# Optimization experiments

Hardware: AMD Instinct MI355X
Metric: run time of the kernel (lower is better)

Reference implementation:

```python
import jax, jax.numpy as jnp
import numpy as np

DIM = 192
HEADS = 8
TIME = 256
HID = int(DIM * 2.66)  # 510
B, H, W = 4, 128, 128


def conv1x1(x, w, b):
    # w: [O, C], pointwise conv as einsum
    return jnp.einsum('bchw,oc->bohw', x, w) + b[None, :, None, None]


def dwconv3(x, w, b):
    # depthwise 3x3, w: [C, 1, 3, 3]
    y = jax.lax.conv_general_dilated(
        x, w, window_strides=(1, 1), padding='SAME',
        feature_group_count=x.shape[1],
        dimension_numbers=('NCHW', 'OIHW', 'NCHW'))
    return y + b[None, :, None, None]


def layernorm(x, w, b, eps=1e-6):
    # channel-wise LN; torch .std() is unbiased (ddof=1)
    C = x.shape[1]
    mean = x.mean(axis=1, keepdims=True)
    var = ((x - mean) ** 2).sum(axis=1, keepdims=True) / (C - 1)
    std = jnp.sqrt(var)
    return w * (x - mean) / (std + eps) + b


def modulate(x, t_emb, tw, tb):
    # time_mlp = Linear(SiLU(t_emb)); scale/shift conditioning
    t = jax.nn.silu(t_emb) @ tw.T + tb  # [B, 2C]
    scale, shift = jnp.split(t, 2, axis=-1)
    return x * (1.0 + scale[:, :, None, None]) + shift[:, :, None, None]


def l2norm(x, eps=1e-12):
    n = jnp.sqrt((x * x).sum(axis=-1, keepdims=True))
    return x / jnp.maximum(n, eps)


def mdta(x, t_emb, temp, qkv_w, qkv_b, dw_w, dw_b, proj_w, proj_b, tw, tb):
    Bn, C, Hh, Ww = x.shape
    x = modulate(x, t_emb, tw, tb)
    qkv = dwconv3(conv1x1(x, qkv_w, qkv_b), dw_w, dw_b)
    q, k, v = jnp.split(qkv, 3, axis=1)
    rs = lambda a: a.reshape(Bn, HEADS, C // HEADS, Hh * Ww)
    q, k, v = l2norm(rs(q)), l2norm(rs(k)), rs(v)
    attn = jnp.einsum('bhcl,bhdl->bhcd', q, k) * temp[None]  # [B,h,c,c]
    attn = jax.nn.softmax(attn, axis=-1)
    out = jnp.einsum('bhcd,bhdl->bhcl', attn, v).reshape(Bn, C, Hh, Ww)
    return conv1x1(out, proj_w, proj_b)


def gdfn(x, t_emb, c1_w, c1_b, dw_w, dw_b, c2_w, c2_b, tw, tb):
    x = modulate(x, t_emb, tw, tb)
    x = dwconv3(conv1x1(x, c1_w, c1_b), dw_w, dw_b)
    x1, x2 = jnp.split(x, 2, axis=1)
    return conv1x1(x1 * x2, c2_w, c2_b)


def setup_inputs() -> dict:
    key = jax.random.key(0)
    ks = jax.random.split(key, 16)
    s = 0.02
    d = {
        'x': jax.random.normal(ks[0], (B, DIM, H, W), jnp.float32),
        't_emb': jax.random.normal(ks[1], (B, TIME), jnp.float32),
        'n1_w': jnp.ones((1, DIM, 1, 1), jnp.float32),
        'n1_b': jnp.zeros((1, DIM, 1, 1), jnp.float32),
        'temp': jnp.ones((HEADS, 1, 1), jnp.float32),
        'a_qkv_w': jax.random.normal(ks[2], (3 * DIM, DIM), jnp.float32) * s,
        'a_qkv_b': jnp.zeros((3 * DIM,), jnp.float32),
        'a_dw_w': jax.random.normal(ks[3], (3 * DIM, 1, 3, 3), jnp.float32) * s,
        'a_dw_b': jnp.zeros((3 * DIM,), jnp.float32),
        'a_proj_w': jax.random.normal(ks[4], (DIM, DIM), jnp.float32) * s,
        'a_proj_b': jnp.zeros((DIM,), jnp.float32),
        'a_t_w': jax.random.normal(ks[5], (2 * DIM, TIME), jnp.float32) * s,
        'a_t_b': jnp.zeros((2 * DIM,), jnp.float32),
        'n2_w': jnp.ones((1, DIM, 1, 1), jnp.float32),
        'n2_b': jnp.zeros((1, DIM, 1, 1), jnp.float32),
        'f_c1_w': jax.random.normal(ks[6], (2 * HID, DIM), jnp.float32) * s,
        'f_c1_b': jnp.zeros((2 * HID,), jnp.float32),
        'f_dw_w': jax.random.normal(ks[7], (2 * HID, 1, 3, 3), jnp.float32) * s,
        'f_dw_b': jnp.zeros((2 * HID,), jnp.float32),
        'f_c2_w': jax.random.normal(ks[8], (DIM, HID), jnp.float32) * s,
        'f_c2_b': jnp.zeros((DIM,), jnp.float32),
        'f_t_w': jax.random.normal(ks[9], (2 * DIM, TIME), jnp.float32) * s,
        'f_t_b': jnp.zeros((2 * DIM,), jnp.float32),
    }
    return d


def reference(x, t_emb, n1_w, n1_b, temp, a_qkv_w, a_qkv_b, a_dw_w, a_dw_b,
              a_proj_w, a_proj_b, a_t_w, a_t_b, n2_w, n2_b,
              f_c1_w, f_c1_b, f_dw_w, f_dw_b, f_c2_w, f_c2_b, f_t_w, f_t_b):
    x = x + mdta(layernorm(x, n1_w, n1_b), t_emb, temp,
                 a_qkv_w, a_qkv_b, a_dw_w, a_dw_b, a_proj_w, a_proj_b, a_t_w, a_t_b)
    x = x + gdfn(layernorm(x, n2_w, n2_b), t_emb,
                 f_c1_w, f_c1_b, f_dw_w, f_dw_b, f_c2_w, f_c2_b, f_t_w, f_t_b)
    return x
```

## Files before the change

### kernel.cpp

```cpp
#include <hip/hip_runtime.h>
#include <math.h>

#define HW 16384

using short8 = __attribute__((ext_vector_type(8))) short;
using f32x4  = __attribute__((ext_vector_type(4))) float;

__device__ __forceinline__ float bf2f(unsigned short u){
  union { unsigned int i; float f; } x; x.i = ((unsigned int)u) << 16; return x.f;
}
__device__ __forceinline__ unsigned short f2bf(float f){
  union { float f; unsigned int i; } x; x.f = f;
  return (unsigned short)((x.i + 0x7FFFu + ((x.i >> 16) & 1u)) >> 16);
}

__global__ void castw_k(const float* __restrict__ in, unsigned short* __restrict__ out, int n){
  int i = blockIdx.x * 256 + threadIdx.x;
  if (i < n) out[i] = f2bf(in[i]);
}
__global__ void castw_pad_k(const float* __restrict__ in, unsigned short* __restrict__ out,
                            int M, int Kin, int Kout){
  int i = blockIdx.x * 256 + threadIdx.x;
  if (i < M * Kout){
    int m = i / Kout, k = i - m * Kout;
    out[i] = (k < Kin) ? f2bf(in[m * Kin + k]) : (unsigned short)0;
  }
}

__global__ void modk(const float* __restrict__ t_emb,
                     const float* __restrict__ aw, const float* __restrict__ ab,
                     const float* __restrict__ fw, const float* __restrict__ fb,
                     float* __restrict__ mod_a, float* __restrict__ mod_f){
  int o = blockIdx.x * 128 + threadIdx.x;
  int b = blockIdx.y;
  const float* w  = blockIdx.z ? fw : aw;
  const float* bi = blockIdx.z ? fb : ab;
  float* outp     = blockIdx.z ? mod_f : mod_a;
  const float* te = t_emb + b * 256;
  float acc = bi[o];
  for (int k = 0; k < 256; ++k){
    float u = te[k];
    float s = u / (1.f + expf(-u));
    acc += s * w[o * 256 + k];
  }
  outp[b * 384 + o] = acc;
}

__global__ __launch_bounds__(256) void lnmod_k(const float* __restrict__ x,
                                               const float* __restrict__ nw, const float* __restrict__ nb,
                                               const float* __restrict__ mod, unsigned short* __restrict__ y){
  int b = blockIdx.y;
  int p = blockIdx.x * 256 + threadIdx.x;
  const float* xb = x + (size_t)b * 192 * HW + p;
  float s = 0.f, s2 = 0.f;
  #pragma unroll 8
  for (int c = 0; c < 192; ++c){
    float v = xb[(size_t)c * HW]; s += v; s2 += v * v;
  }
  float mean = s * (1.f / 192.f);
  float var  = (s2 - s * mean) * (1.f / 191.f);
  float rinv = 1.f / (sqrtf(fmaxf(var, 0.f)) + 1e-6f);
  const float* mo = mod + b * 384;
  unsigned short* yb = y + ((size_t)b * HW + p) * 192;
  #pragma unroll
  for (int c8 = 0; c8 < 24; ++c8){
    unsigned short ob[8];
    #pragma unroll
    for (int j = 0; j < 8; ++j){
      int c = c8 * 8 + j;
      float v = xb[(size_t)c * HW];
      float ln = nw[c] * ((v - mean) * rinv) + nb[c];
      ob[j] = f2bf(ln * (1.f + mo[c]) + mo[192 + c]);
    }
    *(uint4*)(yb + c8 * 8) = *(const uint4*)ob;
  }
}

__global__ __launch_bounds__(256, 2) void gemm_tn2(const unsigned short* __restrict__ A,
                                                   const unsigned short* __restrict__ Bact,
                                                   const float* __restrict__ bias,
                                                   const float* resid, void* outp,
                                                   int M, int K, int nMb, int ofp32){
  const int N = HW;
  __shared__ unsigned short SMEM[20480];
  const int G = gridDim.x;
  const int bid = blockIdx.x;
  const int lb = (bid & 7) * (G >> 3) + (bid >> 3);
  const int mb = lb % nMb;
  const int rest = lb / nMb;
  const int n0 = (rest & 63) * 256;
  const int bz = rest >> 6;
  const unsigned short* Bp = Bact + (size_t)bz * N * K;
  const int m0 = mb * 64;
  const int t = threadIdx.x;
  const int w = t >> 6, lane = t & 63;
  const int l16 = lane & 15, quad = lane >> 4;

  const int arow = t >> 2, akc = t & 3;
  int gm = m0 + arow; if (gm > M - 1) gm = M - 1;
  const unsigned short* agp = A + (size_t)gm * K + akc * 8;
  const int aoff = arow * 32 + ((akc ^ ((arow ^ (arow >> 2)) & 3)) * 8);
  const int brow = t >> 2, bkc = t & 3;
  const unsigned short* bgp = Bp + (size_t)(n0 + brow) * K + bkc * 8;
  const int bslot = (bkc ^ ((brow ^ (brow >> 2)) & 3)) * 8;

  f32x4 acc[4][4];
  #pragma unroll
  for (int i = 0; i < 4; ++i)
    #pragma unroll
    for (int j = 0; j < 4; ++j) acc[i][j] = (f32x4){0.f, 0.f, 0.f, 0.f};

  const int kTiles = K >> 5;
  {
    uint4 va = *(const uint4*)agp;
    *(uint4*)&SMEM[aoff] = va;
    #pragma unroll
    for (int i = 0; i < 4; ++i){
      uint4 vb = *(const uint4*)(bgp + (size_t)(64 * i) * K);
      *(uint4*)&SMEM[4096 + (brow + 64 * i) * 32 + bslot] = vb;
    }
  }
  __syncthreads();

  const int fs = (quad ^ ((l16 ^ (l16 >> 2)) & 3)) * 8;
  for (int kt = 0; kt < kTiles; ++kt){
    const int cur = kt & 1;
    const bool more = (kt + 1 < kTiles);
    uint4 va; uint4 vb[4];
    if (more){
      const int k0 = (kt + 1) * 32;
      va = *(const uint4*)(agp + k0);
      #pragma unroll
      for (int i = 0; i < 4; ++i)
        vb[i] = *(const uint4*)(bgp + (size_t)(64 * i) * K + k0);
    }
    const int abase = cur * 2048;
    const int bbase = 4096 + cur * 8192;
    short8 af[4], bfr[4];
    #pragma unroll
    for (int mt = 0; mt < 4; ++mt)
      af[mt] = *(const short8*)&SMEM[abase + (mt * 16 + l16) * 32 + fs];
    #pragma unroll
    for (int nt = 0; nt < 4; ++nt)
      bfr[nt] = *(const short8*)&SMEM[bbase + (w * 64 + nt * 16 + l16) * 32 + fs];
    #pragma unroll
    for (int nt = 0; nt < 4; ++nt)
      #pragma unroll
      for (int mt = 0; mt < 4; ++mt)
        acc[mt][nt] = __builtin_amdgcn_mfma_f32_16x16x32_bf16(af[mt], bfr[nt], acc[mt][nt], 0, 0, 0);
    if (more){
      const int nabase = (cur ^ 1) * 2048;
      const int nbbase = 4096 + (cur ^ 1) * 8192;
      *(uint4*)&SMEM[nabase + aoff] = va;
      #pragma unroll
      for (int i = 0; i < 4; ++i)
        *(uint4*)&SMEM[nbbase + (brow + 64 * i) * 32 + bslot] = vb[i];
    }
    __syncthreads();
  }

  if (!ofp32){
    unsigned short* T = SMEM;
    #pragma unroll
    for (int mt = 0; mt < 4; ++mt)
      #pragma unroll
      for (int nt = 0; nt < 4; ++nt)
        #pragma unroll
        for (int r = 0; r < 4; ++r){
          int ml = mt * 16 + quad * 4 + r;
          int bm = m0 + ml; if (bm > M - 1) bm = M - 1;
          T[ml * 264 + w * 64 + nt * 16 + l16] = f2bf(acc[mt][nt][r] + bias[bm]);
        }
    __syncthreads();
    unsigned short* ob = (unsigned short*)outp + (size_t)bz * M * N;
    #pragma unroll
    for (int i = 0; i < 8; ++i){
      int c = t + 256 * i;
      int row = c >> 5, col = (c & 31) * 8;
      if (m0 + row < M)
        *(uint4*)(ob + (size_t)(m0 + row) * N + n0 + col) = *(const uint4*)&T[row * 264 + col];
    }
  } else {
    float* T = (float*)&SMEM[0];
    float* ob = (float*)outp + (size_t)bz * M * N;
    const float* rb = resid ? resid + (size_t)bz * M * N : nullptr;
    #pragma unroll
    for (int half = 0; half < 2; ++half){
      #pragma unroll
      for (int mt = 0; mt < 2; ++mt)
        #pragma unroll
        for (int nt = 0; nt < 4; ++nt)
          #pragma unroll
          for (int r = 0; r < 4; ++r){
            int ml = mt * 16 + quad * 4 + r;
            T[ml * 260 + w * 64 + nt * 16 + l16] = acc[half * 2 + mt][nt][r];
          }
      __syncthreads();
      #pragma unroll
      for (int i = 0; i < 8; ++i){
        int c = t + 256 * i;
        int row = c >> 6, col = (c & 63) * 4;
        int m = m0 + half * 32 + row;
        if (m < M){
          size_t idx = (size_t)m * N + n0 + col;
          f32x4 v = *(const f32x4*)&T[row * 260 + col];
          float bv = bias[m];
          v[0] += bv; v[1] += bv; v[2] += bv; v[3] += bv;
          if (rb){
            v[0] += rb[idx]; v[1] += rb[idx + 1]; v[2] += rb[idx + 2]; v[3] += rb[idx + 3];
          }
          *(f32x4*)&ob[idx] = v;
        }
      }
      __syncthreads();
    }
  }
}

__global__ __launch_bounds__(256) void dw3_k(const unsigned short* __restrict__ in,
                                             const float* __restrict__ w, const float* __restrict__ bias,
                                             unsigned short* __restrict__ out, int C,
                                             float* __restrict__ qn, float* __restrict__ kn){
  __shared__ unsigned short tile[66 * 128];
  __shared__ float red[4];
  int zc = blockIdx.y;
  int b = zc / C, c = zc - b * C;
  int r0 = blockIdx.x * 64;
  const unsigned short* im = in + ((size_t)(b * C + c)) * HW;
  unsigned short* om = out + ((size_t)(b * C + c)) * HW;
  int t = threadIdx.x;
  #pragma unroll
  for (int i = 0; i < 5; ++i){
    int idx = t + 256 * i;
    if (idx < 1056){
      int lr = idx >> 4, lc = (idx & 15) * 8;
      int gr = r0 - 1 + lr;
      uint4 v = {0u, 0u, 0u, 0u};
      if ((unsigned)gr < 128u) v = *(const uint4*)(im + gr * 128 + lc);
      *(uint4*)&tile[lr * 128 + lc] = v;
    }
  }
  __syncthreads();
  const float* wc = w + c * 9;
  float W[9];
  #pragma unroll
  for (int i = 0; i < 9; ++i) W[i] = wc[i];
  float bs = bias[c];
  float ssq = 0.f;
  #pragma unroll
  for (int i = 0; i < 4; ++i){
    int seg = t + 256 * i;
    int orow = seg >> 4, sc = (seg & 15) * 8;
    float acc[8];
    #pragma unroll
    for (int j = 0; j < 8; ++j) acc[j] = bs;
    #pragma unroll
    for (int rr = 0; rr < 3; ++rr){
      const unsigned short* rp = &tile[(orow + rr) * 128 + sc];
      float v[10];
      v[0] = (sc > 0) ? bf2f(rp[-1]) : 0.f;
      uint4 m = *(const uint4*)rp;
      const unsigned short* mu = (const unsigned short*)&m;
      #pragma unroll
      for (int j = 0; j < 8; ++j) v[j + 1] = bf2f(mu[j]);
      v[9] = (sc < 120) ? bf2f(rp[8]) : 0.f;
      float wa = W[rr * 3], wb = W[rr * 3 + 1], wd = W[rr * 3 + 2];
      #pragma unroll
      for (int j = 0; j < 8; ++j) acc[j] += wa * v[j] + wb * v[j + 1] + wd * v[j + 2];
    }
    unsigned short ob[8];
    #pragma unroll
    for (int j = 0; j < 8; ++j){
      ob[j] = f2bf(acc[j]);
      float q = bf2f(ob[j]);
      ssq += q * q;
    }
    *(uint4*)(om + (r0 + orow) * 128 + sc) = *(uint4*)ob;
  }
  if (c < 384){
    #pragma unroll
    for (int off = 32; off; off >>= 1) ssq += __shfl_down(ssq, off);
    if ((t & 63) == 0) red[t >> 6] = ssq;
    __syncthreads();
    if (t == 0){
      float s = red[0] + red[1] + red[2] + red[3];
      float* dst = (c < 192) ? (qn + b * 192 + c) : (kn + b * 192 + c - 192);
      atomicAdd(dst, s);
    }
  }
}

__global__ __launch_bounds__(256) void dwgate_k(const unsigned short* __restrict__ h,
                                                const float* __restrict__ w, const float* __restrict__ bias,
                                                unsigned short* __restrict__ g){
  __shared__ unsigned short tile[2 * 66 * 128];
  int zc = blockIdx.y;
  int b = zc / 510, j = zc - b * 510;
  int r0 = blockIdx.x * 64;
  const unsigned short* im1 = h + ((size_t)(b * 1020 + j)) * HW;
  const unsigned short* im2 = h + ((size_t)(b * 1020 + 510 + j)) * HW;
  int t = threadIdx.x;
  #pragma unroll
  for (int i = 0; i < 9; ++i){
    int idx = t + 256 * i;
    if (idx < 2112){
      int img = (idx >= 1056) ? 1 : 0;
      int li = idx - img * 1056;
      int lr = li >> 4, lc = (li & 15) * 8;
      int gr = r0 - 1 + lr;
      uint4 v = {0u, 0u, 0u, 0u};
      const unsigned short* im = img ? im2 : im1;
      if ((unsigned)gr < 128u) v = *(const uint4*)(im + gr * 128 + lc);
      *(uint4*)&tile[img * 8448 + lr * 128 + lc] = v;
    }
  }
  __syncthreads();
  float W1[9], W2[9];
  #pragma unroll
  for (int i = 0; i < 9; ++i){ W1[i] = w[j * 9 + i]; W2[i] = w[(510 + j) * 9 + i]; }
  float b1 = bias[j], b2 = bias[510 + j];
  unsigned short* gm = g + ((size_t)(b * 510 + j)) * HW;
  #pragma unroll
  for (int i = 0; i < 4; ++i){
    int seg = t + 256 * i;
    int orow = seg >> 4, sc = (seg & 15) * 8;
    float a1[8], a2[8];
    #pragma unroll
    for (int q = 0; q < 8; ++q){ a1[q] = b1; a2[q] = b2; }
    #pragma unroll
    for (int rr = 0; rr < 3; ++rr){
      #pragma unroll
      for (int img = 0; img < 2; ++img){
        const unsigned short* rp = &tile[img * 8448 + (orow + rr) * 128 + sc];
        float v[10];
        v[0] = (sc > 0) ? bf2f(rp[-1]) : 0.f;
        uint4 m = *(const uint4*)rp;
        const unsigned short* mu = (const unsigned short*)&m;
        #pragma unroll
        for (int q = 0; q < 8; ++q) v[q + 1] = bf2f(mu[q]);
        v[9] = (sc < 120) ? bf2f(rp[8]) : 0.f;
        const float* ww = img ? W2 : W1;
        float* aa = img ? a2 : a1;
        float wa = ww[rr * 3], wb = ww[rr * 3 + 1], wd = ww[rr * 3 + 2];
        #pragma unroll
        for (int q = 0; q < 8; ++q) aa[q] += wa * v[q] + wb * v[q + 1] + wd * v[q + 2];
      }
    }
    unsigned short ob[8];
    #pragma unroll
    for (int q = 0; q < 8; ++q) ob[q] = f2bf(a1[q] * a2[q]);
    *(uint4*)(gm + (r0 + orow) * 128 + sc) = *(uint4*)ob;
  }
}

__global__ __launch_bounds__(256) void tr_k(const unsigned short* __restrict__ in,
                                            unsigned short* __restrict__ out, int C, int Kout){
  __shared__ unsigned short tile[64 * 72];
  int b = blockIdx.z;
  int p0 = blockIdx.x * 64, c0 = blockIdx.y * 64;
  int t = threadIdx.x;
  #pragma unroll
  for (int i = 0; i < 2; ++i){
    int id = t + 256 * i;
    int ch = id >> 3, pc = (id & 7) * 8;
    uint4 v = {0u, 0u, 0u, 0u};
    if (c0 + ch < C) v = *(const uint4*)(in + ((size_t)(b * C + c0 + ch)) * HW + p0 + pc);
    const unsigned short* u = (const unsigned short*)&v;
    #pragma unroll
    for (int j = 0; j < 8; ++j) tile[(pc + j) * 72 + ch] = u[j];
  }
  __syncthreads();
  #pragma unroll
  for (int i = 0; i < 2; ++i){
    int id = t + 256 * i;
    int px = id >> 3, cc = (id & 7) * 8;
    *(uint4*)(out + ((size_t)b * HW + p0 + px) * Kout + c0 + cc) = *(const uint4*)&tile[px * 72 + cc];
  }
}

__global__ __launch_bounds__(64) void qk_k(const unsigned short* __restrict__ qkv_dw, float* __restrict__ part){
  int bh = blockIdx.y; int b = bh >> 3, h = bh & 7;
  int ks = blockIdx.x;
  int lane = threadIdx.x;
  int l16 = lane & 15, quad = lane >> 4;
  const unsigned short* qb = qkv_dw + ((size_t)b * 576 + h * 24) * HW;
  const unsigned short* kb = qkv_dw + ((size_t)b * 576 + 192 + h * 24) * HW;
  f32x4 z = {0.f, 0.f, 0.f, 0.f};
  f32x4 a00 = z, a01 = z, a10 = z, a11 = z;
  for (int st = 0; st < 16; ++st){
    int k0 = ks * 512 + st * 32 + quad * 8;
    short8 qa0 = *(const short8*)(qb + (size_t)l16 * HW + k0);
    short8 qa1 = *(const short8*)(qb + (size_t)(l16 + 16) * HW + k0);
    short8 kb0 = *(const short8*)(kb + (size_t)l16 * HW + k0);
    short8 kb1 = *(const short8*)(kb + (size_t)(l16 + 16) * HW + k0);
    a00 = __builtin_amdgcn_mfma_f32_16x16x32_bf16(qa0, kb0, a00, 0, 0, 0);
    a01 = __builtin_amdgcn_mfma_f32_16x16x32_bf16(qa0, kb1, a01, 0, 0, 0);
    a10 = __builtin_amdgcn_mfma_f32_16x16x32_bf16(qa1, kb0, a10, 0, 0, 0);
    a11 = __builtin_amdgcn_mfma_f32_16x16x32_bf16(qa1, kb1, a11, 0, 0, 0);
  }
  float* pp = part + ((size_t)bh * 32 + ks) * 576;
  #pragma unroll
  for (int r = 0; r < 4; ++r){
    int c0 = quad * 4 + r, c1 = 16 + quad * 4 + r;
    int d0 = l16, d1 = 16 + l16;
    if (c0 < 24 && d0 < 24) pp[c0 * 24 + d0] = a00[r];
    if (c0 < 24 && d1 < 24) pp[c0 * 24 + d1] = a01[r];
    if (c1 < 24 && d0 < 24) pp[c1 * 24 + d0] = a10[r];
    if (c1 < 24 && d1 < 24) pp[c1 * 24 + d1] = a11[r];
  }
}

__global__ void softmax_k(const float* __restrict__ part, const float* __restrict__ qn,
                          const float* __restrict__ kn, const float* __restrict__ temp,
                          float* __restrict__ attn){
  int bh = blockIdx.x; int b = bh >> 3, h = bh & 7;
  int c = threadIdx.x;
  if (c >= 24) return;
  float tmp = temp[h];
  float qv = fmaxf(sqrtf(qn[b * 192 + h * 24 + c]), 1e-12f);
  float row[24];
  #pragma unroll
  for (int d = 0; d < 24; ++d){
    float s = 0.f;
    for (int sp = 0; sp < 32; ++sp) s += part[((size_t)bh * 32 + sp) * 576 + c * 24 + d];
    float kv = fmaxf(sqrtf(kn[b * 192 + h * 24 + d]), 1e-12f);
    row[d] = s * tmp / (qv * kv);
  }
  float mx = row[0];
  #pragma unroll
  for (int d = 1; d < 24; ++d) mx = fmaxf(mx, row[d]);
  float sum = 0.f;
  #pragma unroll
  for (int d = 0; d < 24; ++d){ row[d] = expf(row[d] - mx); sum += row[d]; }
  float inv = 1.f / sum;
  #pragma unroll
  for (int d = 0; d < 24; ++d) attn[(size_t)bh * 576 + c * 24 + d] = row[d] * inv;
}

__global__ __launch_bounds__(256) void av_k(const float* __restrict__ attn,
                                            const unsigned short* __restrict__ qkv_dw,
                                            unsigned short* __restrict__ o){
  int bh = blockIdx.y; int b = bh >> 3, h = bh & 7;
  __shared__ float As[576];
  int t = threadIdx.x;
  for (int i = t; i < 576; i += 256) As[i] = attn[(size_t)bh * 576 + i];
  __syncthreads();
  int p = blockIdx.x * 256 + t;
  const unsigned short* vb = qkv_dw + ((size_t)b * 576 + 384 + h * 24) * HW + p;
  float acc[24];
  #pragma unroll
  for (int c = 0; c < 24; ++c) acc[c] = 0.f;
  #pragma unroll
  for (int d = 0; d < 24; ++d){
    float vv = bf2f(vb[(size_t)d * HW]);
    #pragma unroll
    for (int c = 0; c < 24; ++c) acc[c] += As[c * 24 + d] * vv;
  }
  unsigned short ob[24];
  #pragma unroll
  for (int c = 0; c < 24; ++c) ob[c] = f2bf(acc[c]);
  unsigned short* op = o + ((size_t)b * HW + p) * 192 + h * 24;
  #pragma unroll
  for (int i = 0; i < 3; ++i) *(uint4*)(op + i * 8) = *(const uint4*)(ob + i * 8);
}

extern "C" void kernel_launch(void* const* d_in, const int* in_sizes, int n_in,
                              void* d_out, int out_size, void* d_ws, size_t ws_size,
                              hipStream_t stream){
  (void)in_sizes; (void)n_in; (void)out_size; (void)ws_size;
  const float* x        = (const float*)d_in[0];
  const float* t_emb    = (const float*)d_in[1];
  const float* n1_w     = (const float*)d_in[2];
  const float* n1_b     = (const float*)d_in[3];
  const float* temp     = (const float*)d_in[4];
  const float* a_qkv_w  = (const float*)d_in[5];
  const float* a_qkv_b  = (const float*)d_in[6];
  const float* a_dw_w   = (const float*)d_in[7];
  const float* a_dw_b   = (const float*)d_in[8];
  const float* a_proj_w = (const float*)d_in[9];
  const float* a_proj_b = (const float*)d_in[10];
  const float* a_t_w    = (const float*)d_in[11];
  const float* a_t_b    = (const float*)d_in[12];
  const float* n2_w     = (const float*)d_in[13];
  const float* n2_b     = (const float*)d_in[14];
  const float* f_c1_w   = (const float*)d_in[15];
  const float* f_c1_b   = (const float*)d_in[16];
  const float* f_dw_w   = (const float*)d_in[17];
  const float* f_dw_b   = (const float*)d_in[18];
  const float* f_c2_w   = (const float*)d_in[19];
  const float* f_c2_b   = (const float*)d_in[20];
  const float* f_t_w    = (const float*)d_in[21];
  const float* f_t_b    = (const float*)d_in[22];
  float* out = (float*)d_out;
  char* ws = (char*)d_ws;

  unsigned short* y_buf = (unsigned short*)(ws + 0);
  unsigned short* qkv   = (unsigned short*)(ws + 25165824);
  unsigned short* hbuf  = (unsigned short*)(ws + 25165824);
  unsigned short* gbufT = (unsigned short*)(ws + 25165824);
  unsigned short* qkvd  = (unsigned short*)(ws + 100663296);
  unsigned short* obuf  = (unsigned short*)(ws + 176160768);
  unsigned short* gbuf  = (unsigned short*)(ws + 158859264);
  const size_t S = 225705984;
  float* mod_a = (float*)(ws + S);
  float* mod_f = (float*)(ws + S + 8192);
  float* qn    = (float*)(ws + S + 16384);
  float* kn    = (float*)(ws + S + 20480);
  float* part  = (float*)(ws + S + 24576);
  float* attn  = (float*)(ws + S + 2383872);
  unsigned short* Wq  = (unsigned short*)(ws + S + 2457600);
  unsigned short* Wp  = (unsigned short*)(ws + S + 2678784);
  unsigned short* W1  = (unsigned short*)(ws + S + 2752512);
  unsigned short* W2p = (unsigned short*)(ws + S + 3144192);

  castw_k<<<dim3((110592 + 255) / 256), 256, 0, stream>>>(a_qkv_w, Wq, 110592);
  castw_k<<<dim3((36864 + 255) / 256), 256, 0, stream>>>(a_proj_w, Wp, 36864);
  castw_k<<<dim3((195840 + 255) / 256), 256, 0, stream>>>(f_c1_w, W1, 195840);
  castw_pad_k<<<dim3((98304 + 255) / 256), 256, 0, stream>>>(f_c2_w, W2p, 192, 510, 512);
  modk<<<dim3(3, 4, 2), 128, 0, stream>>>(t_emb, a_t_w, a_t_b, f_t_w, f_t_b, mod_a, mod_f);
  (void)hipMemsetAsync(qn, 0, 2 * 768 * sizeof(float), stream);

  lnmod_k<<<dim3(64, 4), 256, 0, stream>>>(x, n1_w, n1_b, mod_a, y_buf);
  gemm_tn2<<<2304, 256, 0, stream>>>(Wq, y_buf, a_qkv_b, nullptr, qkv, 576, 192, 9, 0);
  dw3_k<<<dim3(2, 2304), 256, 0, stream>>>(qkv, a_dw_w, a_dw_b, qkvd, 576, qn, kn);
  qk_k<<<dim3(32, 32), 64, 0, stream>>>(qkvd, part);
  softmax_k<<<32, 64, 0, stream>>>(part, qn, kn, temp, attn);
  av_k<<<dim3(64, 32), 256, 0, stream>>>(attn, qkvd, obuf);
  gemm_tn2<<<768, 256, 0, stream>>>(Wp, obuf, a_proj_b, x, out, 192, 192, 3, 1);

  lnmod_k<<<dim3(64, 4), 256, 0, stream>>>(out, n2_w, n2_b, mod_f, y_buf);
  gemm_tn2<<<4096, 256, 0, stream>>>(W1, y_buf, f_c1_b, nullptr, hbuf, 1020, 192, 16, 0);
  dwgate_k<<<dim3(2, 2040), 256, 0, stream>>>(hbuf, f_dw_w, f_dw_b, gbuf);
  tr_k<<<dim3(256, 8, 4), 256, 0, stream>>>(gbuf, gbufT, 510, 512);
  gemm_tn2<<<768, 256, 0, stream>>>(W2p, gbufT, f_c2_b, out, out, 192, 512, 3, 1);
}
```

Baseline: 741.4 us.

## Fuse channel-major transpose into final GEMM B-tile loads, drop tr_k

```diff
diff --git a/kernel.cpp b/kernel.cpp
--- a/kernel.cpp
+++ b/kernel.cpp
@@ -76,6 +76,7 @@
   }
 }
 
+template<int CMAJ>
 __global__ __launch_bounds__(256, 2) void gemm_tn2(const unsigned short* __restrict__ A,
                                                    const unsigned short* __restrict__ Bact,
                                                    const float* __restrict__ bias,
@@ -90,7 +91,6 @@
   const int rest = lb / nMb;
   const int n0 = (rest & 63) * 256;
   const int bz = rest >> 6;
-  const unsigned short* Bp = Bact + (size_t)bz * N * K;
   const int m0 = mb * 64;
   const int t = threadIdx.x;
   const int w = t >> 6, lane = t & 63;
@@ -100,9 +100,16 @@
   int gm = m0 + arow; if (gm > M - 1) gm = M - 1;
   const unsigned short* agp = A + (size_t)gm * K + akc * 8;
   const int aoff = arow * 32 + ((akc ^ ((arow ^ (arow >> 2)) & 3)) * 8);
+
+  const unsigned short* Bp;
   const int brow = t >> 2, bkc = t & 3;
-  const unsigned short* bgp = Bp + (size_t)(n0 + brow) * K + bkc * 8;
-  const int bslot = (bkc ^ ((brow ^ (brow >> 2)) & 3)) * 8;
+  int bslot = 0;
+  if (CMAJ == 0){
+    Bp = Bact + (size_t)bz * N * K;
+    bslot = (bkc ^ ((brow ^ (brow >> 2)) & 3)) * 8;
+  } else {
+    Bp = Bact + (size_t)bz * CMAJ * HW;
+  }
 
   f32x4 acc[4][4];
   #pragma unroll
@@ -112,12 +119,27 @@
 
   const int kTiles = K >> 5;
   {
-    uint4 va = *(const uint4*)agp;
-    *(uint4*)&SMEM[aoff] = va;
-    #pragma unroll
-    for (int i = 0; i < 4; ++i){
-      uint4 vb = *(const uint4*)(bgp + (size_t)(64 * i) * K);
-      *(uint4*)&SMEM[4096 + (brow + 64 * i) * 32 + bslot] = vb;
+    *(uint4*)&SMEM[aoff] = *(const uint4*)agp;
+    if (CMAJ == 0){
+      const unsigned short* bgp = Bp + (size_t)(n0 + brow) * K + bkc * 8;
+      #pragma unroll
+      for (int i = 0; i < 4; ++i)
+        *(uint4*)&SMEM[4096 + (brow + 64 * i) * 32 + bslot] = *(const uint4*)(bgp + (size_t)(64 * i) * K);
+    } else {
+      #pragma unroll
+      for (int i = 0; i < 4; ++i){
+        int id = t + 256 * i;
+        int chl = id >> 5, po = (id & 31) * 8;
+        int cg = chl; if (cg > CMAJ - 1) cg = CMAJ - 1;
+        uint4 v = *(const uint4*)(Bp + (size_t)cg * HW + n0 + po);
+        const unsigned short* u = (const unsigned short*)&v;
+        #pragma unroll
+        for (int j = 0; j < 8; ++j){
+          int px = po + j;
+          int phys = (chl >> 3) ^ ((px ^ (px >> 2)) & 3);
+          SMEM[4096 + px * 32 + phys * 8 + (chl & 7)] = u[j];
+        }
+      }
     }
   }
   __syncthreads();
@@ -130,9 +152,20 @@
     if (more){
       const int k0 = (kt + 1) * 32;
       va = *(const uint4*)(agp + k0);
-      #pragma unroll
-      for (int i = 0; i < 4; ++i)
-        vb[i] = *(const uint4*)(bgp + (size_t)(64 * i) * K + k0);
+      if (CMAJ == 0){
+        const unsigned short* bgp = Bp + (size_t)(n0 + brow) * K + bkc * 8;
+        #pragma unroll
+        for (int i = 0; i < 4; ++i)
+          vb[i] = *(const uint4*)(bgp + (size_t)(64 * i) * K + k0);
+      } else {
+        #pragma unroll
+        for (int i = 0; i < 4; ++i){
+          int id = t + 256 * i;
+          int chl = id >> 5;
+          int cg = k0 + chl; if (cg > CMAJ - 1) cg = CMAJ - 1;
+          vb[i] = *(const uint4*)(Bp + (size_t)cg * HW + n0 + (id & 31) * 8);
+        }
+      }
     }
     const int abase = cur * 2048;
     const int bbase = 4096 + cur * 8192;
@@ -152,9 +185,24 @@
       const int nabase = (cur ^ 1) * 2048;
       const int nbbase = 4096 + (cur ^ 1) * 8192;
       *(uint4*)&SMEM[nabase + aoff] = va;
-      #pragma unroll
-      for (int i = 0; i < 4; ++i)
-        *(uint4*)&SMEM[nbbase + (brow + 64 * i) * 32 + bslot] = vb[i];
+      if (CMAJ == 0){
+        #pragma unroll
+        for (int i = 0; i < 4; ++i)
+          *(uint4*)&SMEM[nbbase + (brow + 64 * i) * 32 + bslot] = vb[i];
+      } else {
+        #pragma unroll
+        for (int i = 0; i < 4; ++i){
+          int id = t + 256 * i;
+          int chl = id >> 5, po = (id & 31) * 8;
+          const unsigned short* u = (const unsigned short*)&vb[i];
+          #pragma unroll
+          for (int j = 0; j < 8; ++j){
+            int px = po + j;
+            int phys = (chl >> 3) ^ ((px ^ (px >> 2)) & 3);
+            SMEM[nbbase + px * 32 + phys * 8 + (chl & 7)] = u[j];
+          }
+        }
+      }
     }
     __syncthreads();
   }
@@ -350,31 +398,6 @@
     #pragma unroll
     for (int q = 0; q < 8; ++q) ob[q] = f2bf(a1[q] * a2[q]);
     *(uint4*)(gm + (r0 + orow) * 128 + sc) = *(uint4*)ob;
-  }
-}
-
-__global__ __launch_bounds__(256) void tr_k(const unsigned short* __restrict__ in,
-                                            unsigned short* __restrict__ out, int C, int Kout){
-  __shared__ unsigned short tile[64 * 72];
-  int b = blockIdx.z;
-  int p0 = blockIdx.x * 64, c0 = blockIdx.y * 64;
-  int t = threadIdx.x;
-  #pragma unroll
-  for (int i = 0; i < 2; ++i){
-    int id = t + 256 * i;
-    int ch = id >> 3, pc = (id & 7) * 8;
-    uint4 v = {0u, 0u, 0u, 0u};
-    if (c0 + ch < C) v = *(const uint4*)(in + ((size_t)(b * C + c0 + ch)) * HW + p0 + pc);
-    const unsigned short* u = (const unsigned short*)&v;
-    #pragma unroll
-    for (int j = 0; j < 8; ++j) tile[(pc + j) * 72 + ch] = u[j];
-  }
-  __syncthreads();
-  #pragma unroll
-  for (int i = 0; i < 2; ++i){
-    int id = t + 256 * i;
-    int px = id >> 3, cc = (id & 7) * 8;
-    *(uint4*)(out + ((size_t)b * HW + p0 + px) * Kout + c0 + cc) = *(const uint4*)&tile[px * 72 + cc];
   }
 }
 
@@ -497,7 +520,6 @@
   unsigned short* y_buf = (unsigned short*)(ws + 0);
   unsigned short* qkv   = (unsigned short*)(ws + 25165824);
   unsigned short* hbuf  = (unsigned short*)(ws + 25165824);
-  unsigned short* gbufT = (unsigned short*)(ws + 25165824);
   unsigned short* qkvd  = (unsigned short*)(ws + 100663296);
   unsigned short* obuf  = (unsigned short*)(ws + 176160768);
   unsigned short* gbuf  = (unsigned short*)(ws + 158859264);
@@ -521,16 +543,15 @@
   (void)hipMemsetAsync(qn, 0, 2 * 768 * sizeof(float), stream);
 
   lnmod_k<<<dim3(64, 4), 256, 0, stream>>>(x, n1_w, n1_b, mod_a, y_buf);
-  gemm_tn2<<<2304, 256, 0, stream>>>(Wq, y_buf, a_qkv_b, nullptr, qkv, 576, 192, 9, 0);
+  gemm_tn2<0><<<2304, 256, 0, stream>>>(Wq, y_buf, a_qkv_b, nullptr, qkv, 576, 192, 9, 0);
   dw3_k<<<dim3(2, 2304), 256, 0, stream>>>(qkv, a_dw_w, a_dw_b, qkvd, 576, qn, kn);
   qk_k<<<dim3(32, 32), 64, 0, stream>>>(qkvd, part);
   softmax_k<<<32, 64, 0, stream>>>(part, qn, kn, temp, attn);
   av_k<<<dim3(64, 32), 256, 0, stream>>>(attn, qkvd, obuf);
-  gemm_tn2<<<768, 256, 0, stream>>>(Wp, obuf, a_proj_b, x, out, 192, 192, 3, 1);
+  gemm_tn2<0><<<768, 256, 0, stream>>>(Wp, obuf, a_proj_b, x, out, 192, 192, 3, 1);
 
   lnmod_k<<<dim3(64, 4), 256, 0, stream>>>(out, n2_w, n2_b, mod_f, y_buf);
-  gemm_tn2<<<4096, 256, 0, stream>>>(W1, y_buf, f_c1_b, nullptr, hbuf, 1020, 192, 16, 0);
+  gemm_tn2<0><<<4096, 256, 0, stream>>>(W1, y_buf, f_c1_b, nullptr, hbuf, 1020, 192, 16, 0);
   dwgate_k<<<dim3(2, 2040), 256, 0, stream>>>(hbuf, f_dw_w, f_dw_b, gbuf);
-  tr_k<<<dim3(256, 8, 4), 256, 0, stream>>>(gbuf, gbufT, 510, 512);
-  gemm_tn2<<<768, 256, 0, stream>>>(W2p, gbufT, f_c2_b, out, out, 192, 512, 3, 1);
-}
+  gemm_tn2<510><<<768, 256, 0, stream>>>(W2p, gbuf, f_c2_b, out, out, 192, 512, 3, 1);
+}
```

Result: no change. 739.6 us (-0.2%).
